# Performance work log

Measured on AMD Instinct MI355X. Metric: run time of the kernel, lower is better.

Reference implementation:

```python
import jax, jax.numpy as jnp
import numpy as np

B, S, H, E, K = 4, 2048, 1024, 8, 2


def setup_inputs() -> dict:
    key = jax.random.key(0)
    k_hs, k_eo, k_w1, k_w2 = jax.random.split(key, 4)
    return {
        "hidden_states": jax.random.normal(k_hs, (B, S, H), dtype=jnp.float32),
        "expert_outputs": jax.random.normal(k_eo, (E, B, S, H), dtype=jnp.float32),
        "W1": jax.random.normal(k_w1, (H, H), dtype=jnp.float32) * 0.02,
        "b1": jnp.zeros((H,), dtype=jnp.float32),
        "W2": jax.random.normal(k_w2, (H, E), dtype=jnp.float32) * 0.02,
        "b2": jnp.zeros((E,), dtype=jnp.float32),
        "k": K,
    }


def reference(hidden_states, expert_outputs, W1, b1, W2, b2, k):
    # Router MLP (eval mode: dropout is identity, no noise)
    h = jax.nn.relu(hidden_states @ W1 + b1)          # [B,S,H]
    router_logits = h @ W2 + b2                        # [B,S,E]
    router_probs = jax.nn.softmax(router_logits, axis=-1)
    top_k_gates, top_k_indices = jax.lax.top_k(router_probs, k)  # [B,S,k]
    n_experts = expert_outputs.shape[0]
    # Scatter top-k gates into a dense [B,S,E] gate matrix (same math as the
    # per-expert masked accumulation in the torch loop)
    onehot = jax.nn.one_hot(top_k_indices, n_experts, dtype=top_k_gates.dtype)  # [B,S,k,E]
    gate_mat = jnp.einsum('bsk,bske->bse', top_k_gates, onehot)
    combined = jnp.einsum('bse,ebsd->bsd', gate_mat, expert_outputs)
    return combined
```

## Files before the change

kernel.cpp:

```cpp
#include <hip/hip_runtime.h>
#include <math.h>


#define H_DIM 1024
#define E_NUM 8

typedef __attribute__((ext_vector_type(8))) short s16x8;
typedef __attribute__((ext_vector_type(8))) unsigned short u16x8;
typedef __attribute__((ext_vector_type(4))) float f32x4;

__device__ __forceinline__ unsigned short f2bf(float x) {
    unsigned int u = __float_as_uint(x);
    unsigned int r = (u + 0x7FFFu + ((u >> 16) & 1u)) >> 16;
    return (unsigned short)r;
}
__device__ __forceinline__ float bf2f(unsigned short b) {
    return __uint_as_float(((unsigned int)b) << 16);
}
__device__ __forceinline__ void gload_lds16(const void* g, void* lds) {
    __builtin_amdgcn_global_load_lds(
        (const __attribute__((address_space(1))) void*)g,
        (__attribute__((address_space(3))) void*)lds, 16, 0, 0);
}

__global__ __launch_bounds__(256) void prep_fused_kernel(
    const float* __restrict__ A, const float* __restrict__ W,
    char* __restrict__ Aimg, char* __restrict__ Bimg)
{
    if (blockIdx.x < 4096) {
        int t = blockIdx.x * 256 + threadIdx.x;
        int m = t >> 7;
        int k = (t & 127) << 3;
        const float* src = A + ((size_t)m << 10) + k;
        float4 v0 = *reinterpret_cast<const float4*>(src);
        float4 v1 = *reinterpret_cast<const float4*>(src + 4);
        float xs[8] = {v0.x, v0.y, v0.z, v0.w, v1.x, v1.y, v1.z, v1.w};
        u16x8 hv, lv;
        #pragma unroll
        for (int j = 0; j < 8; ++j) {
            unsigned short h = f2bf(xs[j]);
            hv[j] = h;
            lv[j] = f2bf(xs[j] - bf2f(h));
        }
        int rb = m >> 7, mr = m & 127, kt = k >> 5, s = (k >> 3) & 3;
        char* base = Aimg + (((size_t)(rb * 32 + kt)) << 14) + mr * 128;
        *reinterpret_cast<u16x8*>(base + ((s ^ (mr & 7)) << 4)) = hv;
        *reinterpret_cast<u16x8*>(base + (((s + 4) ^ (mr & 7)) << 4)) = lv;
    } else {
        int t = (blockIdx.x - 4096) * 256 + threadIdx.x;
        int n = t & 1023;
        int k = (t >> 10) << 3;
        u16x8 hv, lv;
        #pragma unroll
        for (int j = 0; j < 8; ++j) {
            float x = W[((size_t)(k + j) << 10) + n];
            unsigned short h = f2bf(x);
            hv[j] = h;
            lv[j] = f2bf(x - bf2f(h));
        }
        int cb = n >> 7, nr = n & 127, kt = k >> 5, s = (k >> 3) & 3;
        char* base = Bimg + (((size_t)(cb * 32 + kt)) << 14) + nr * 128;
        *reinterpret_cast<u16x8*>(base + ((s ^ (nr & 7)) << 4)) = hv;
        *reinterpret_cast<u16x8*>(base + (((s + 4) ^ (nr & 7)) << 4)) = lv;
    }
}

#define MFMA_B16 __builtin_amdgcn_mfma_f32_16x16x32_bf16

__global__ __launch_bounds__(256, 3) void gemm1_mfma_kernel(
    const char* __restrict__ Aimg, const char* __restrict__ Bimg,
    const float* __restrict__ bias, float* __restrict__ Hout)
{
    __shared__ char As[16384];
    __shared__ char Bs[16384];

    int bid = blockIdx.x;
    int swz = (bid & 7) * 64 + (bid >> 3);
    int rb = swz >> 3;
    int cb = swz & 7;

    int tid = threadIdx.x;
    int lane = tid & 63;
    int wave = tid >> 6;
    int wm = (wave >> 1) * 64;
    int wn = (wave & 1) * 64;
    int l15 = lane & 15, l4 = lane >> 4;

    int aoff_h[4], aoff_l[4], boff_h[4], boff_l[4];
    #pragma unroll
    for (int f = 0; f < 4; ++f) {
        int ar = wm + f * 16 + l15;
        aoff_h[f] = ar * 128 + ((l4 ^ (ar & 7)) << 4);
        aoff_l[f] = ar * 128 + (((l4 + 4) ^ (ar & 7)) << 4);
        int br = wn + f * 16 + l15;
        boff_h[f] = br * 128 + ((l4 ^ (br & 7)) << 4);
        boff_l[f] = br * 128 + (((l4 + 4) ^ (br & 7)) << 4);
    }

    const char* abase = Aimg + (size_t)rb * (32 * 16384);
    const char* bbase = Bimg + (size_t)cb * (32 * 16384);

    f32x4 acc[4][4];
    #pragma unroll
    for (int i = 0; i < 4; ++i)
        #pragma unroll
        for (int j = 0; j < 4; ++j)
            acc[i][j] = (f32x4){0.f, 0.f, 0.f, 0.f};

    for (int kt = 0; kt < 32; ++kt) {
        const char* ga = abase + (kt << 14);
        const char* gb = bbase + (kt << 14);
        int toff = tid << 4;
        #pragma unroll
        for (int r = 0; r < 4; ++r) {
            gload_lds16(ga + (r << 12) + toff, As + (r << 12) + toff);
            gload_lds16(gb + (r << 12) + toff, Bs + (r << 12) + toff);
        }
        __syncthreads();

        s16x8 ah[4], al[4], bh[4], bl[4];
        #pragma unroll
        for (int f = 0; f < 4; ++f) {
            ah[f] = *reinterpret_cast<const s16x8*>(As + aoff_h[f]);
            al[f] = *reinterpret_cast<const s16x8*>(As + aoff_l[f]);
            bh[f] = *reinterpret_cast<const s16x8*>(Bs + boff_h[f]);
            bl[f] = *reinterpret_cast<const s16x8*>(Bs + boff_l[f]);
        }
        #pragma unroll
        for (int m = 0; m < 4; ++m)
            #pragma unroll
            for (int n = 0; n < 4; ++n)
                acc[m][n] = MFMA_B16(ah[m], bh[n], acc[m][n], 0, 0, 0);
        #pragma unroll
        for (int m = 0; m < 4; ++m)
            #pragma unroll
            for (int n = 0; n < 4; ++n)
                acc[m][n] = MFMA_B16(ah[m], bl[n], acc[m][n], 0, 0, 0);
        #pragma unroll
        for (int m = 0; m < 4; ++m)
            #pragma unroll
            for (int n = 0; n < 4; ++n)
                acc[m][n] = MFMA_B16(al[m], bh[n], acc[m][n], 0, 0, 0);
        __syncthreads();
    }

    int row0 = rb * 128 + wm;
    int col0 = cb * 128 + wn;
    float bcol[4];
    #pragma unroll
    for (int fn = 0; fn < 4; ++fn) bcol[fn] = bias[col0 + fn * 16 + l15];
    #pragma unroll
    for (int fm = 0; fm < 4; ++fm)
        #pragma unroll
        for (int r = 0; r < 4; ++r) {
            int row = row0 + fm * 16 + l4 * 4 + r;
            float* orow = Hout + ((size_t)row << 10);
            #pragma unroll
            for (int fn = 0; fn < 4; ++fn) {
                int col = col0 + fn * 16 + l15;
                orow[col] = fmaxf(acc[fm][fn][r] + bcol[fn], 0.f);
            }
        }
}

#define BM 128
#define BN 128
#define BK 16
#define PAD_LD 132

__global__ __launch_bounds__(256) void gemm1_relu_kernel(
    const float* __restrict__ A, const float* __restrict__ W,
    const float* __restrict__ bias, float* __restrict__ Hout,
    int M, int N, int K)
{
    __shared__ float As[BK][PAD_LD];
    __shared__ float Bs[BK][PAD_LD];
    const int tid = threadIdx.x;
    const int tx = tid & 15;
    const int ty = tid >> 4;
    const int row0 = blockIdx.y * BM;
    const int col0 = blockIdx.x * BN;
    float acc[8][8];
    #pragma unroll
    for (int i = 0; i < 8; ++i)
        #pragma unroll
        for (int j = 0; j < 8; ++j) acc[i][j] = 0.f;
    const int a_row = tid >> 2;
    const int a_k4  = (tid & 3) * 4;
    const int b_col4 = (tid & 31) * 4;
    const int b_kk   = tid >> 5;
    for (int k0 = 0; k0 < K; k0 += BK) {
        #pragma unroll
        for (int half = 0; half < 2; ++half) {
            int r = a_row + half * 64;
            float4 av = *reinterpret_cast<const float4*>(&A[(size_t)(row0 + r) * K + k0 + a_k4]);
            As[a_k4 + 0][r] = av.x; As[a_k4 + 1][r] = av.y;
            As[a_k4 + 2][r] = av.z; As[a_k4 + 3][r] = av.w;
        }
        #pragma unroll
        for (int half = 0; half < 2; ++half) {
            int kk = b_kk + half * 8;
            float4 bv = *reinterpret_cast<const float4*>(&W[(size_t)(k0 + kk) * N + col0 + b_col4]);
            *reinterpret_cast<float4*>(&Bs[kk][b_col4]) = bv;
        }
        __syncthreads();
        #pragma unroll
        for (int k = 0; k < BK; ++k) {
            float4 a0 = *reinterpret_cast<const float4*>(&As[k][ty * 8]);
            float4 a1 = *reinterpret_cast<const float4*>(&As[k][ty * 8 + 4]);
            float4 b0 = *reinterpret_cast<const float4*>(&Bs[k][tx * 8]);
            float4 b1 = *reinterpret_cast<const float4*>(&Bs[k][tx * 8 + 4]);
            float a[8] = {a0.x, a0.y, a0.z, a0.w, a1.x, a1.y, a1.z, a1.w};
            float b[8] = {b0.x, b0.y, b0.z, b0.w, b1.x, b1.y, b1.z, b1.w};
            #pragma unroll
            for (int i = 0; i < 8; ++i)
                #pragma unroll
                for (int j = 0; j < 8; ++j)
                    acc[i][j] = fmaf(a[i], b[j], acc[i][j]);
        }
        __syncthreads();
    }
    #pragma unroll
    for (int i = 0; i < 8; ++i) {
        int row = row0 + ty * 8 + i;
        #pragma unroll
        for (int j4 = 0; j4 < 2; ++j4) {
            int col = col0 + tx * 8 + j4 * 4;
            float4 v;
            v.x = fmaxf(acc[i][j4 * 4 + 0] + bias[col + 0], 0.f);
            v.y = fmaxf(acc[i][j4 * 4 + 1] + bias[col + 1], 0.f);
            v.z = fmaxf(acc[i][j4 * 4 + 2] + bias[col + 2], 0.f);
            v.w = fmaxf(acc[i][j4 * 4 + 3] + bias[col + 3], 0.f);
            *reinterpret_cast<float4*>(&Hout[(size_t)row * N + col]) = v;
        }
    }
}

__global__ __launch_bounds__(256) void route_combine_kernel(
    const float* __restrict__ Hbuf, const float* __restrict__ W2,
    const float* __restrict__ b2, const float* __restrict__ EO,
    float* __restrict__ Out, int M)
{
    const int t = blockIdx.x;
    const int tid = threadIdx.x;
    const int lane = tid & 63;
    const int wave = tid >> 6;
    const float* hrow = Hbuf + (size_t)t * H_DIM;

    float part[E_NUM];
    #pragma unroll
    for (int e = 0; e < E_NUM; ++e) part[e] = 0.f;
    #pragma unroll
    for (int it = 0; it < H_DIM / 256; ++it) {
        int j = tid + it * 256;
        float hv = hrow[j];
        const float* w = W2 + (size_t)j * E_NUM;
        #pragma unroll
        for (int e = 0; e < E_NUM; ++e) part[e] = fmaf(hv, w[e], part[e]);
    }
    #pragma unroll
    for (int off = 32; off > 0; off >>= 1)
        #pragma unroll
        for (int e = 0; e < E_NUM; ++e)
            part[e] += __shfl_down(part[e], off, 64);

    __shared__ float sred[4][E_NUM];
    __shared__ float s_g[2];
    __shared__ int   s_e[2];
    if (lane == 0)
        #pragma unroll
        for (int e = 0; e < E_NUM; ++e) sred[wave][e] = part[e];
    __syncthreads();

    if (tid == 0) {
        float logits[E_NUM];
        #pragma unroll
        for (int e = 0; e < E_NUM; ++e)
            logits[e] = sred[0][e] + sred[1][e] + sred[2][e] + sred[3][e] + b2[e];
        float m = logits[0];
        #pragma unroll
        for (int e = 1; e < E_NUM; ++e) m = fmaxf(m, logits[e]);
        float p[E_NUM], ssum = 0.f;
        #pragma unroll
        for (int e = 0; e < E_NUM; ++e) { p[e] = expf(logits[e] - m); ssum += p[e]; }
        float inv = 1.f / ssum;
        #pragma unroll
        for (int e = 0; e < E_NUM; ++e) p[e] *= inv;
        int e0 = 0;
        #pragma unroll
        for (int e = 1; e < E_NUM; ++e) if (p[e] > p[e0]) e0 = e;
        int e1 = (e0 == 0) ? 1 : 0;
        #pragma unroll
        for (int e = 0; e < E_NUM; ++e)
            if (e != e0 && e != e1 && p[e] > p[e1]) e1 = e;
        s_g[0] = p[e0]; s_g[1] = p[e1];
        s_e[0] = e0;    s_e[1] = e1;
    }
    __syncthreads();

    const float g0 = s_g[0], g1 = s_g[1];
    const size_t base0 = ((size_t)s_e[0] * M + t) * H_DIM;
    const size_t base1 = ((size_t)s_e[1] * M + t) * H_DIM;
    const int d = tid * 4;
    float4 x0 = *reinterpret_cast<const float4*>(&EO[base0 + d]);
    float4 x1 = *reinterpret_cast<const float4*>(&EO[base1 + d]);
    float4 o;
    o.x = g0 * x0.x + g1 * x1.x;
    o.y = g0 * x0.y + g1 * x1.y;
    o.z = g0 * x0.z + g1 * x1.z;
    o.w = g0 * x0.w + g1 * x1.w;
    *reinterpret_cast<float4*>(&Out[(size_t)t * H_DIM + d]) = o;
}

extern "C" void kernel_launch(void* const* d_in, const int* in_sizes, int n_in,
                              void* d_out, int out_size, void* d_ws, size_t ws_size,
                              hipStream_t stream)
{
    const float* hs = (const float*)d_in[0];
    const float* EO = (const float*)d_in[1];
    const float* W1 = (const float*)d_in[2];
    const float* b1 = (const float*)d_in[3];
    const float* W2 = (const float*)d_in[4];
    const float* b2 = (const float*)d_in[5];

    const int M = in_sizes[0] / H_DIM;
    float* out = (float*)d_out;

    const size_t A_IMG = (size_t)64 * 32 * 16384;
    const size_t B_IMG = (size_t)8 * 32 * 16384;
    if (M == 8192 && ws_size >= A_IMG + B_IMG) {
        char* Aimg = (char*)d_ws;
        char* Bimg = (char*)d_ws + A_IMG;
        prep_fused_kernel<<<4096 + 512, 256, 0, stream>>>(hs, W1, Aimg, Bimg);
        gemm1_mfma_kernel<<<512, 256, 0, stream>>>(Aimg, Bimg, b1, out);
    } else {
        dim3 grid1(H_DIM / BN, M / BM);
        gemm1_relu_kernel<<<grid1, 256, 0, stream>>>(hs, W1, b1, out, M, H_DIM, H_DIM);
    }
    route_combine_kernel<<<M, 256, 0, stream>>>(out, W2, b2, EO, out, M);
}
```

Baseline: 86.56 us.

## Fuse router second GEMM into first GEMM epilogue, emitting partial logits

The first GEMM kernel no longer writes the full [M,H] ReLU activation to global memory. Each block converts its ReLU tile to split bf16 in LDS and multiplies it with a bf16-split slice of W2 on MFMA, writing per-column-block partial logits. A new combine kernel sums the eight partials, adds the bias and performs softmax, top-2 and the expert combine. This removes the 32 MB H write and read, at the cost of extra LDS, a larger epilogue with more syncs, and a small partial-logit buffer.

```diff
diff --git a/kernel.cpp b/kernel.cpp
--- a/kernel.cpp
+++ b/kernel.cpp
@@ -66,13 +66,15 @@
 }
 
 #define MFMA_B16 __builtin_amdgcn_mfma_f32_16x16x32_bf16
-
-__global__ __launch_bounds__(256, 3) void gemm1_mfma_kernel(
+#define W2T_OFS 32768
+#define W2T_PITCH 272
+
+__global__ __launch_bounds__(256, 3) void gemm1_logits_kernel(
     const char* __restrict__ Aimg, const char* __restrict__ Bimg,
-    const float* __restrict__ bias, float* __restrict__ Hout)
-{
-    __shared__ char As[16384];
-    __shared__ char Bs[16384];
+    const float* __restrict__ bias, const float* __restrict__ W2,
+    float* __restrict__ Plog)
+{
+    __shared__ char smem[39296];
 
     int bid = blockIdx.x;
     int swz = (bid & 7) * 64 + (bid >> 3);
@@ -86,6 +88,24 @@
     int wn = (wave & 1) * 64;
     int l15 = lane & 15, l4 = lane >> 4;
 
+    const int col0g = cb * 128;
+    for (int i = tid; i < 1632; i += 256)
+        *reinterpret_cast<float*>(smem + W2T_OFS + i * 4) = 0.f;
+    __syncthreads();
+    {
+        int e = tid & 7, c4 = tid >> 3;
+        #pragma unroll
+        for (int j = 0; j < 4; ++j) {
+            int col = c4 * 4 + j;
+            float w = W2[(size_t)(col0g + col) * E_NUM + e];
+            unsigned short wh = f2bf(w);
+            unsigned short wl = f2bf(w - bf2f(wh));
+            *reinterpret_cast<unsigned short*>(smem + W2T_OFS + e * W2T_PITCH + col * 2) = wh;
+            *reinterpret_cast<unsigned short*>(smem + W2T_OFS + (e + 8) * W2T_PITCH + col * 2) = wl;
+        }
+    }
+    __syncthreads();
+
     int aoff_h[4], aoff_l[4], boff_h[4], boff_l[4];
     #pragma unroll
     for (int f = 0; f < 4; ++f) {
@@ -93,8 +113,8 @@
         aoff_h[f] = ar * 128 + ((l4 ^ (ar & 7)) << 4);
         aoff_l[f] = ar * 128 + (((l4 + 4) ^ (ar & 7)) << 4);
         int br = wn + f * 16 + l15;
-        boff_h[f] = br * 128 + ((l4 ^ (br & 7)) << 4);
-        boff_l[f] = br * 128 + (((l4 + 4) ^ (br & 7)) << 4);
+        boff_h[f] = 16384 + br * 128 + ((l4 ^ (br & 7)) << 4);
+        boff_l[f] = 16384 + br * 128 + (((l4 + 4) ^ (br & 7)) << 4);
     }
 
     const char* abase = Aimg + (size_t)rb * (32 * 16384);
@@ -113,18 +133,18 @@
         int toff = tid << 4;
         #pragma unroll
         for (int r = 0; r < 4; ++r) {
-            gload_lds16(ga + (r << 12) + toff, As + (r << 12) + toff);
-            gload_lds16(gb + (r << 12) + toff, Bs + (r << 12) + toff);
+            gload_lds16(ga + (r << 12) + toff, smem + (r << 12) + toff);
+            gload_lds16(gb + (r << 12) + toff, smem + 16384 + (r << 12) + toff);
         }
         __syncthreads();
 
         s16x8 ah[4], al[4], bh[4], bl[4];
         #pragma unroll
         for (int f = 0; f < 4; ++f) {
-            ah[f] = *reinterpret_cast<const s16x8*>(As + aoff_h[f]);
-            al[f] = *reinterpret_cast<const s16x8*>(As + aoff_l[f]);
-            bh[f] = *reinterpret_cast<const s16x8*>(Bs + boff_h[f]);
-            bl[f] = *reinterpret_cast<const s16x8*>(Bs + boff_l[f]);
+            ah[f] = *reinterpret_cast<const s16x8*>(smem + aoff_h[f]);
+            al[f] = *reinterpret_cast<const s16x8*>(smem + aoff_l[f]);
+            bh[f] = *reinterpret_cast<const s16x8*>(smem + boff_h[f]);
+            bl[f] = *reinterpret_cast<const s16x8*>(smem + boff_l[f]);
         }
         #pragma unroll
         for (int m = 0; m < 4; ++m)
@@ -144,139 +164,93 @@
         __syncthreads();
     }
 
-    int row0 = rb * 128 + wm;
-    int col0 = cb * 128 + wn;
     float bcol[4];
     #pragma unroll
-    for (int fn = 0; fn < 4; ++fn) bcol[fn] = bias[col0 + fn * 16 + l15];
-    #pragma unroll
-    for (int fm = 0; fm < 4; ++fm)
-        #pragma unroll
-        for (int r = 0; r < 4; ++r) {
-            int row = row0 + fm * 16 + l4 * 4 + r;
-            float* orow = Hout + ((size_t)row << 10);
-            #pragma unroll
-            for (int fn = 0; fn < 4; ++fn) {
-                int col = col0 + fn * 16 + l15;
-                orow[col] = fmaxf(acc[fm][fn][r] + bcol[fn], 0.f);
+    for (int fn = 0; fn < 4; ++fn) bcol[fn] = bias[col0g + wn + fn * 16 + l15];
+
+    f32x4 plog[2];
+    plog[0] = (f32x4){0.f, 0.f, 0.f, 0.f};
+    plog[1] = (f32x4){0.f, 0.f, 0.f, 0.f};
+
+    #pragma unroll
+    for (int ch = 0; ch < 2; ++ch) {
+        if ((wave & 1) == ch) {
+            #pragma unroll
+            for (int fm = 0; fm < 4; ++fm)
+                #pragma unroll
+                for (int r = 0; r < 4; ++r) {
+                    int row = wm + fm * 16 + l4 * 4 + r;
+                    int rx = (row & 7) << 4;
+                    #pragma unroll
+                    for (int fn = 0; fn < 4; ++fn) {
+                        float hv = fmaxf(acc[fm][fn][r] + bcol[fn], 0.f);
+                        unsigned short hh = f2bf(hv);
+                        unsigned short hl = f2bf(hv - bf2f(hh));
+                        int byteoff = row * 128 + ((((fn * 16 + l15) * 2)) ^ rx);
+                        *reinterpret_cast<unsigned short*>(smem + byteoff) = hh;
+                        *reinterpret_cast<unsigned short*>(smem + 16384 + byteoff) = hl;
+                    }
+                }
+        }
+        __syncthreads();
+
+        #pragma unroll
+        for (int fmm = 0; fmm < 2; ++fmm) {
+            int rowb = wave * 32 + fmm * 16 + l15;
+            int rx = (rowb & 7) << 4;
+            int rowbase = rowb * 128;
+            #pragma unroll
+            for (int kc = 0; kc < 2; ++kc) {
+                int co = kc * 64 + l4 * 16;
+                s16x8 ahi = *reinterpret_cast<const s16x8*>(smem + rowbase + (co ^ rx));
+                s16x8 alo = *reinterpret_cast<const s16x8*>(smem + 16384 + rowbase + (co ^ rx));
+                int wb = W2T_OFS + ch * 128 + kc * 64 + l4 * 16;
+                s16x8 whi = *reinterpret_cast<const s16x8*>(smem + wb + l15 * W2T_PITCH);
+                s16x8 wlo = *reinterpret_cast<const s16x8*>(smem + wb + (l15 + 8) * W2T_PITCH);
+                plog[fmm] = MFMA_B16(ahi, whi, plog[fmm], 0, 0, 0);
+                plog[fmm] = MFMA_B16(ahi, wlo, plog[fmm], 0, 0, 0);
+                plog[fmm] = MFMA_B16(alo, whi, plog[fmm], 0, 0, 0);
             }
         }
-}
-
-#define BM 128
-#define BN 128
-#define BK 16
-#define PAD_LD 132
-
-__global__ __launch_bounds__(256) void gemm1_relu_kernel(
-    const float* __restrict__ A, const float* __restrict__ W,
-    const float* __restrict__ bias, float* __restrict__ Hout,
-    int M, int N, int K)
-{
-    __shared__ float As[BK][PAD_LD];
-    __shared__ float Bs[BK][PAD_LD];
-    const int tid = threadIdx.x;
-    const int tx = tid & 15;
-    const int ty = tid >> 4;
-    const int row0 = blockIdx.y * BM;
-    const int col0 = blockIdx.x * BN;
-    float acc[8][8];
-    #pragma unroll
-    for (int i = 0; i < 8; ++i)
-        #pragma unroll
-        for (int j = 0; j < 8; ++j) acc[i][j] = 0.f;
-    const int a_row = tid >> 2;
-    const int a_k4  = (tid & 3) * 4;
-    const int b_col4 = (tid & 31) * 4;
-    const int b_kk   = tid >> 5;
-    for (int k0 = 0; k0 < K; k0 += BK) {
-        #pragma unroll
-        for (int half = 0; half < 2; ++half) {
-            int r = a_row + half * 64;
-            float4 av = *reinterpret_cast<const float4*>(&A[(size_t)(row0 + r) * K + k0 + a_k4]);
-            As[a_k4 + 0][r] = av.x; As[a_k4 + 1][r] = av.y;
-            As[a_k4 + 2][r] = av.z; As[a_k4 + 3][r] = av.w;
-        }
-        #pragma unroll
-        for (int half = 0; half < 2; ++half) {
-            int kk = b_kk + half * 8;
-            float4 bv = *reinterpret_cast<const float4*>(&W[(size_t)(k0 + kk) * N + col0 + b_col4]);
-            *reinterpret_cast<float4*>(&Bs[kk][b_col4]) = bv;
-        }
-        __syncthreads();
-        #pragma unroll
-        for (int k = 0; k < BK; ++k) {
-            float4 a0 = *reinterpret_cast<const float4*>(&As[k][ty * 8]);
-            float4 a1 = *reinterpret_cast<const float4*>(&As[k][ty * 8 + 4]);
-            float4 b0 = *reinterpret_cast<const float4*>(&Bs[k][tx * 8]);
-            float4 b1 = *reinterpret_cast<const float4*>(&Bs[k][tx * 8 + 4]);
-            float a[8] = {a0.x, a0.y, a0.z, a0.w, a1.x, a1.y, a1.z, a1.w};
-            float b[8] = {b0.x, b0.y, b0.z, b0.w, b1.x, b1.y, b1.z, b1.w};
-            #pragma unroll
-            for (int i = 0; i < 8; ++i)
-                #pragma unroll
-                for (int j = 0; j < 8; ++j)
-                    acc[i][j] = fmaf(a[i], b[j], acc[i][j]);
-        }
-        __syncthreads();
-    }
-    #pragma unroll
-    for (int i = 0; i < 8; ++i) {
-        int row = row0 + ty * 8 + i;
-        #pragma unroll
-        for (int j4 = 0; j4 < 2; ++j4) {
-            int col = col0 + tx * 8 + j4 * 4;
-            float4 v;
-            v.x = fmaxf(acc[i][j4 * 4 + 0] + bias[col + 0], 0.f);
-            v.y = fmaxf(acc[i][j4 * 4 + 1] + bias[col + 1], 0.f);
-            v.z = fmaxf(acc[i][j4 * 4 + 2] + bias[col + 2], 0.f);
-            v.w = fmaxf(acc[i][j4 * 4 + 3] + bias[col + 3], 0.f);
-            *reinterpret_cast<float4*>(&Hout[(size_t)row * N + col]) = v;
-        }
-    }
-}
-
-__global__ __launch_bounds__(256) void route_combine_kernel(
-    const float* __restrict__ Hbuf, const float* __restrict__ W2,
-    const float* __restrict__ b2, const float* __restrict__ EO,
-    float* __restrict__ Out, int M)
+        __syncthreads();
+    }
+
+    if (l15 < 8) {
+        #pragma unroll
+        for (int fmm = 0; fmm < 2; ++fmm) {
+            int rowg = rb * 128 + wave * 32 + fmm * 16 + l4 * 4;
+            #pragma unroll
+            for (int r = 0; r < 4; ++r)
+                Plog[((size_t)cb * 8192 + rowg + r) * E_NUM + l15] = plog[fmm][r];
+        }
+    }
+}
+
+__global__ __launch_bounds__(256) void route_combine2_kernel(
+    const float* __restrict__ Plog, const float* __restrict__ b2,
+    const float* __restrict__ EO, float* __restrict__ Out, int M)
 {
     const int t = blockIdx.x;
     const int tid = threadIdx.x;
-    const int lane = tid & 63;
-    const int wave = tid >> 6;
-    const float* hrow = Hbuf + (size_t)t * H_DIM;
-
-    float part[E_NUM];
-    #pragma unroll
-    for (int e = 0; e < E_NUM; ++e) part[e] = 0.f;
-    #pragma unroll
-    for (int it = 0; it < H_DIM / 256; ++it) {
-        int j = tid + it * 256;
-        float hv = hrow[j];
-        const float* w = W2 + (size_t)j * E_NUM;
-        #pragma unroll
-        for (int e = 0; e < E_NUM; ++e) part[e] = fmaf(hv, w[e], part[e]);
-    }
-    #pragma unroll
-    for (int off = 32; off > 0; off >>= 1)
-        #pragma unroll
-        for (int e = 0; e < E_NUM; ++e)
-            part[e] += __shfl_down(part[e], off, 64);
-
-    __shared__ float sred[4][E_NUM];
+
+    __shared__ float s_logit[E_NUM];
     __shared__ float s_g[2];
     __shared__ int   s_e[2];
-    if (lane == 0)
-        #pragma unroll
-        for (int e = 0; e < E_NUM; ++e) sred[wave][e] = part[e];
+
+    if (tid < 64) {
+        int cbi = tid >> 3, e = tid & 7;
+        float v = Plog[((size_t)cbi * M + t) * E_NUM + e];
+        v += __shfl_xor(v, 8, 64);
+        v += __shfl_xor(v, 16, 64);
+        v += __shfl_xor(v, 32, 64);
+        if (tid < 8) s_logit[tid] = v + b2[tid];
+    }
     __syncthreads();
 
     if (tid == 0) {
         float logits[E_NUM];
         #pragma unroll
-        for (int e = 0; e < E_NUM; ++e)
-            logits[e] = sred[0][e] + sred[1][e] + sred[2][e] + sred[3][e] + b2[e];
+        for (int e = 0; e < E_NUM; ++e) logits[e] = s_logit[e];
         float m = logits[0];
         #pragma unroll
         for (int e = 1; e < E_NUM; ++e) m = fmaxf(m, logits[e]);
@@ -312,6 +286,155 @@
     *reinterpret_cast<float4*>(&Out[(size_t)t * H_DIM + d]) = o;
 }
 
+#define BM 128
+#define BN 128
+#define BK 16
+#define PAD_LD 132
+
+__global__ __launch_bounds__(256) void gemm1_relu_kernel(
+    const float* __restrict__ A, const float* __restrict__ W,
+    const float* __restrict__ bias, float* __restrict__ Hout,
+    int M, int N, int K)
+{
+    __shared__ float As[BK][PAD_LD];
+    __shared__ float Bs[BK][PAD_LD];
+    const int tid = threadIdx.x;
+    const int tx = tid & 15;
+    const int ty = tid >> 4;
+    const int row0 = blockIdx.y * BM;
+    const int col0 = blockIdx.x * BN;
+    float acc[8][8];
+    #pragma unroll
+    for (int i = 0; i < 8; ++i)
+        #pragma unroll
+        for (int j = 0; j < 8; ++j) acc[i][j] = 0.f;
+    const int a_row = tid >> 2;
+    const int a_k4  = (tid & 3) * 4;
+    const int b_col4 = (tid & 31) * 4;
+    const int b_kk   = tid >> 5;
+    for (int k0 = 0; k0 < K; k0 += BK) {
+        #pragma unroll
+        for (int half = 0; half < 2; ++half) {
+            int r = a_row + half * 64;
+            float4 av = *reinterpret_cast<const float4*>(&A[(size_t)(row0 + r) * K + k0 + a_k4]);
+            As[a_k4 + 0][r] = av.x; As[a_k4 + 1][r] = av.y;
+            As[a_k4 + 2][r] = av.z; As[a_k4 + 3][r] = av.w;
+        }
+        #pragma unroll
+        for (int half = 0; half < 2; ++half) {
+            int kk = b_kk + half * 8;
+            float4 bv = *reinterpret_cast<const float4*>(&W[(size_t)(k0 + kk) * N + col0 + b_col4]);
+            *reinterpret_cast<float4*>(&Bs[kk][b_col4]) = bv;
+        }
+        __syncthreads();
+        #pragma unroll
+        for (int k = 0; k < BK; ++k) {
+            float4 a0 = *reinterpret_cast<const float4*>(&As[k][ty * 8]);
+            float4 a1 = *reinterpret_cast<const float4*>(&As[k][ty * 8 + 4]);
+            float4 b0 = *reinterpret_cast<const float4*>(&Bs[k][tx * 8]);
+            float4 b1 = *reinterpret_cast<const float4*>(&Bs[k][tx * 8 + 4]);
+            float a[8] = {a0.x, a0.y, a0.z, a0.w, a1.x, a1.y, a1.z, a1.w};
+            float b[8] = {b0.x, b0.y, b0.z, b0.w, b1.x, b1.y, b1.z, b1.w};
+            #pragma unroll
+            for (int i = 0; i < 8; ++i)
+                #pragma unroll
+                for (int j = 0; j < 8; ++j)
+                    acc[i][j] = fmaf(a[i], b[j], acc[i][j]);
+        }
+        __syncthreads();
+    }
+    #pragma unroll
+    for (int i = 0; i < 8; ++i) {
+        int row = row0 + ty * 8 + i;
+        #pragma unroll
+        for (int j4 = 0; j4 < 2; ++j4) {
+            int col = col0 + tx * 8 + j4 * 4;
+            float4 v;
+            v.x = fmaxf(acc[i][j4 * 4 + 0] + bias[col + 0], 0.f);
+            v.y = fmaxf(acc[i][j4 * 4 + 1] + bias[col + 1], 0.f);
+            v.z = fmaxf(acc[i][j4 * 4 + 2] + bias[col + 2], 0.f);
+            v.w = fmaxf(acc[i][j4 * 4 + 3] + bias[col + 3], 0.f);
+            *reinterpret_cast<float4*>(&Hout[(size_t)row * N + col]) = v;
+        }
+    }
+}
+
+__global__ __launch_bounds__(256) void route_combine_kernel(
+    const float* __restrict__ Hbuf, const float* __restrict__ W2,
+    const float* __restrict__ b2, const float* __restrict__ EO,
+    float* __restrict__ Out, int M)
+{
+    const int t = blockIdx.x;
+    const int tid = threadIdx.x;
+    const int lane = tid & 63;
+    const int wave = tid >> 6;
+    const float* hrow = Hbuf + (size_t)t * H_DIM;
+
+    float part[E_NUM];
+    #pragma unroll
+    for (int e = 0; e < E_NUM; ++e) part[e] = 0.f;
+    #pragma unroll
+    for (int it = 0; it < H_DIM / 256; ++it) {
+        int j = tid + it * 256;
+        float hv = hrow[j];
+        const float* w = W2 + (size_t)j * E_NUM;
+        #pragma unroll
+        for (int e = 0; e < E_NUM; ++e) part[e] = fmaf(hv, w[e], part[e]);
+    }
+    #pragma unroll
+    for (int off = 32; off > 0; off >>= 1)
+        #pragma unroll
+        for (int e = 0; e < E_NUM; ++e)
+            part[e] += __shfl_down(part[e], off, 64);
+
+    __shared__ float sred[4][E_NUM];
+    __shared__ float s_g[2];
+    __shared__ int   s_e[2];
+    if (lane == 0)
+        #pragma unroll
+        for (int e = 0; e < E_NUM; ++e) sred[wave][e] = part[e];
+    __syncthreads();
+
+    if (tid == 0) {
+        float logits[E_NUM];
+        #pragma unroll
+        for (int e = 0; e < E_NUM; ++e)
+            logits[e] = sred[0][e] + sred[1][e] + sred[2][e] + sred[3][e] + b2[e];
+        float m = logits[0];
+        #pragma unroll
+        for (int e = 1; e < E_NUM; ++e) m = fmaxf(m, logits[e]);
+        float p[E_NUM], ssum = 0.f;
+        #pragma unroll
+        for (int e = 0; e < E_NUM; ++e) { p[e] = expf(logits[e] - m); ssum += p[e]; }
+        float inv = 1.f / ssum;
+        #pragma unroll
+        for (int e = 0; e < E_NUM; ++e) p[e] *= inv;
+        int e0 = 0;
+        #pragma unroll
+        for (int e = 1; e < E_NUM; ++e) if (p[e] > p[e0]) e0 = e;
+        int e1 = (e0 == 0) ? 1 : 0;
+        #pragma unroll
+        for (int e = 0; e < E_NUM; ++e)
+            if (e != e0 && e != e1 && p[e] > p[e1]) e1 = e;
+        s_g[0] = p[e0]; s_g[1] = p[e1];
+        s_e[0] = e0;    s_e[1] = e1;
+    }
+    __syncthreads();
+
+    const float g0 = s_g[0], g1 = s_g[1];
+    const size_t base0 = ((size_t)s_e[0] * M + t) * H_DIM;
+    const size_t base1 = ((size_t)s_e[1] * M + t) * H_DIM;
+    const int d = tid * 4;
+    float4 x0 = *reinterpret_cast<const float4*>(&EO[base0 + d]);
+    float4 x1 = *reinterpret_cast<const float4*>(&EO[base1 + d]);
+    float4 o;
+    o.x = g0 * x0.x + g1 * x1.x;
+    o.y = g0 * x0.y + g1 * x1.y;
+    o.z = g0 * x0.z + g1 * x1.z;
+    o.w = g0 * x0.w + g1 * x1.w;
+    *reinterpret_cast<float4*>(&Out[(size_t)t * H_DIM + d]) = o;
+}
+
 extern "C" void kernel_launch(void* const* d_in, const int* in_sizes, int n_in,
                               void* d_out, int out_size, void* d_ws, size_t ws_size,
                               hipStream_t stream)
@@ -328,14 +451,17 @@
 
     const size_t A_IMG = (size_t)64 * 32 * 16384;
     const size_t B_IMG = (size_t)8 * 32 * 16384;
-    if (M == 8192 && ws_size >= A_IMG + B_IMG) {
-        char* Aimg = (char*)d_ws;
-        char* Bimg = (char*)d_ws + A_IMG;
+    const size_t PART  = (size_t)8 * 8192 * 8 * 4;
+    if (M == 8192 && ws_size >= A_IMG + B_IMG + PART) {
+        char*  Aimg = (char*)d_ws;
+        char*  Bimg = (char*)d_ws + A_IMG;
+        float* Plog = (float*)((char*)d_ws + A_IMG + B_IMG);
         prep_fused_kernel<<<4096 + 512, 256, 0, stream>>>(hs, W1, Aimg, Bimg);
-        gemm1_mfma_kernel<<<512, 256, 0, stream>>>(Aimg, Bimg, b1, out);
+        gemm1_logits_kernel<<<512, 256, 0, stream>>>(Aimg, Bimg, b1, W2, Plog);
+        route_combine2_kernel<<<M, 256, 0, stream>>>(Plog, b2, EO, out, M);
     } else {
         dim3 grid1(H_DIM / BN, M / BM);
         gemm1_relu_kernel<<<grid1, 256, 0, stream>>>(hs, W1, b1, out, M, H_DIM, H_DIM);
-    }
-    route_combine_kernel<<<M, 256, 0, stream>>>(out, W2, b2, EO, out, M);
-}
+        route_combine_kernel<<<M, 256, 0, stream>>>(out, W2, b2, EO, out, M);
+    }
+}
```

Measured after the change: 82.53 us, median of 3. 4.7% less time.
